# Kernel optimization log

Measured on AMD Instinct MI355X. Metric: run time of the kernel, lower is better.

The kernel has to match this reference:

```python
import jax, jax.numpy as jnp
import numpy as np

MAX_WEIGHT = 10.0  # config.max_weight
EPS = 1e-8

BATCH = 2048
VOCAB = 256
SEQ_LEN = 64
NUM_DENDRITES = SEQ_LEN * VOCAB  # 16384


def setup_inputs() -> dict:
    key = jax.random.key(0)
    k1, k2 = jax.random.split(key)
    # binary dendrite activations in {0,1}, stored as float32 as in the torch module
    binary = jax.random.randint(k1, (BATCH, NUM_DENDRITES), 0, 2).astype(jnp.float32)
    # raw_weights ~ Uniform(-1, 1) per nn.init.uniform_
    raw_weights = jax.random.uniform(k2, (VOCAB, NUM_DENDRITES), dtype=jnp.float32,
                                     minval=-1.0, maxval=1.0)
    return {"binary": binary, "raw_weights": raw_weights}


def reference(binary, raw_weights):
    # bounded positive weights: max_weight * sigmoid(raw)
    w = MAX_WEIGHT * jax.nn.sigmoid(raw_weights)            # (vocab, D)
    log_w = jnp.log(jnp.clip(w, EPS))                       # (vocab, D)
    # masked log-sum: where binary==0 the torch code uses log(1)=0, then multiplies
    # by binary anyway, so it is exactly binary @ log_w.T
    log_sum = jnp.einsum('bd,vd->bv', binary, log_w)        # (batch, vocab)
    n_active = jnp.clip(jnp.sum(binary, axis=-1, keepdims=True), 1.0)  # (batch, 1)
    logits = jnp.exp(log_sum / n_active)                    # geometric mean of fired weights
    return logits
```

## Files before the change

### kernel.cpp

```cpp
#include <hip/hip_runtime.h>

#define BATCH 2048
#define VOCAB 256
#define KDIM 16384
#define BM 64
#define BK 64
#define S_SPLIT 32
#define KCHUNK (KDIM / S_SPLIT)
#define NT (KCHUNK / BK)
#define LN10 2.302585092994046f

typedef __attribute__((ext_vector_type(8))) short short8;
typedef __attribute__((ext_vector_type(4))) float f32x4;

#define FENCE asm volatile("" ::: "memory")

__device__ __forceinline__ unsigned short f2bf_rne(float f) {
  unsigned int u = __float_as_uint(f);
  u += 0x7fffu + ((u >> 16) & 1u);
  return (unsigned short)(u >> 16);
}
__device__ __forceinline__ unsigned int pack2(float lo, float hi) {
  return (__float_as_uint(lo) >> 16) | (__float_as_uint(hi) & 0xffff0000u);
}

__device__ __forceinline__ void async16(void* lds, const void* g) {
  __builtin_amdgcn_global_load_lds(
      (const __attribute__((address_space(1))) unsigned int*)g,
      (__attribute__((address_space(3))) unsigned int*)lds, 16, 0, 0);
}

__global__ __launch_bounds__(256) void k_logw(const float* __restrict__ raw,
                                              unsigned short* __restrict__ logw) {
  int i = blockIdx.x * 256 + threadIdx.x;
  float4 x = ((const float4*)raw)[i];
  ushort4 r;
  r.x = f2bf_rne(LN10 - log1pf(expf(-x.x)));
  r.y = f2bf_rne(LN10 - log1pf(expf(-x.y)));
  r.z = f2bf_rne(LN10 - log1pf(expf(-x.z)));
  r.w = f2bf_rne(LN10 - log1pf(expf(-x.w)));
  ((ushort4*)logw)[i] = r;
}

template <int PART>
__global__ __launch_bounds__(256, 3) void k_gemm(
    const float* __restrict__ binary, const unsigned short* __restrict__ logw,
    float* __restrict__ outp, float* __restrict__ nactp) {
  __shared__ char smem[40960];
  char* const Asm = smem;
  char* const Bsm = smem + 8192;

  const int tid = threadIdx.x;
  const int wv = tid >> 6;
  const int lane = tid & 63;
  const int l15 = lane & 15;
  const int lhi = lane >> 4;
  const int sx = blockIdx.x;
  const int my = blockIdx.y;
  const int m0 = my * BM;
  const int k0 = sx * KCHUNK;

  const int ar = tid >> 2, ac = tid & 3;
  const float* asrc = binary + (size_t)(m0 + ar) * KDIM + k0 + ac * 16;
  const int ar7 = ar & 7;
  const int aw0 = ar * 128 + ((((ac * 2) ^ ar7) << 4));
  const int aw1 = ar * 128 + ((((ac * 2 + 1) ^ ar7) << 4));

  const unsigned short* bsrc =
      logw + (size_t)(wv * 64 + (lane >> 3)) * KDIM + k0 +
      (((lane & 7) ^ (lane >> 3)) << 3);

  const int rsw = (l15 & 7) << 4;

  f32x4 acc[4][4];
#pragma unroll
  for (int m = 0; m < 4; ++m)
#pragma unroll
    for (int n = 0; n < 4; ++n) acc[m][n] = f32x4{0.f, 0.f, 0.f, 0.f};
  float asum = 0.f;
  float4 Ra[4], Rb[4];

  auto ALOAD = [&](int t, float4* R) {
    const float4* p = (const float4*)(asrc + t * BK);
    R[0] = p[0]; R[1] = p[1]; R[2] = p[2]; R[3] = p[3];
  };
  auto BSTAGE = [&](int t) {
#pragma unroll
    for (int i = 0; i < 8; ++i)
      async16(Bsm + (wv * 64 + i * 8) * 128, bsrc + (size_t)i * 8 * KDIM + t * BK);
  };
  auto AWRITE = [&](const float4* R) {
#pragma unroll
    for (int j = 0; j < 4; ++j)
      asum += R[j].x + R[j].y + R[j].z + R[j].w;
    uint4 u0, u1;
    u0.x = pack2(R[0].x, R[0].y); u0.y = pack2(R[0].z, R[0].w);
    u0.z = pack2(R[1].x, R[1].y); u0.w = pack2(R[1].z, R[1].w);
    u1.x = pack2(R[2].x, R[2].y); u1.y = pack2(R[2].z, R[2].w);
    u1.z = pack2(R[3].x, R[3].y); u1.w = pack2(R[3].z, R[3].w);
    *(uint4*)(Asm + aw0) = u0;
    *(uint4*)(Asm + aw1) = u1;
  };
  auto COMPUTE = [&]() {
#pragma unroll
    for (int ks = 0; ks < 2; ++ks) {
      const int koff = ((ks * 64) | (lhi * 16)) ^ rsw;
      short8 af[4], bf[4];
#pragma unroll
      for (int m = 0; m < 4; ++m)
        af[m] = *(const short8*)(Asm + (m * 16 + l15) * 128 + koff);
#pragma unroll
      for (int n = 0; n < 4; ++n)
        bf[n] = *(const short8*)(Bsm + (wv * 64 + n * 16 + l15) * 128 + koff);
#pragma unroll
      for (int m = 0; m < 4; ++m)
#pragma unroll
        for (int n = 0; n < 4; ++n)
          acc[m][n] = __builtin_amdgcn_mfma_f32_16x16x32_bf16(bf[n], af[m],
                                                              acc[m][n], 0, 0, 0);
    }
  };

#define VMW4 asm volatile("s_waitcnt vmcnt(4) lgkmcnt(0)" ::: "memory")
#define BAR __builtin_amdgcn_s_barrier()

  ALOAD(0, Ra);
#pragma unroll 1
  for (int t = 0; t < NT; t += 2) {
    BSTAGE(t);
    AWRITE(Ra);
    ALOAD(t + 1, Rb);
    VMW4; BAR; FENCE;
    COMPUTE();
    FENCE; BAR; FENCE;
    BSTAGE(t + 1);
    AWRITE(Rb);
    ALOAD(t + 2 < NT ? t + 2 : NT - 1, Ra);
    VMW4; BAR; FENCE;
    COMPUTE();
    FENCE; BAR; FENCE;
  }

  float s = asum;
  s += __shfl_xor(s, 1, 64);
  s += __shfl_xor(s, 2, 64);

  if (PART) {
    if (ac == 0) nactp[sx * BATCH + m0 + ar] = s;
#pragma unroll
    for (int m = 0; m < 4; ++m) {
      float* dst = outp + ((size_t)sx * BATCH + m0 + m * 16 + l15) * VOCAB +
                   wv * 64 + lhi * 4;
#pragma unroll
      for (int n = 0; n < 4; ++n)
        *(float4*)(dst + n * 16) =
            (float4){acc[m][n][0], acc[m][n][1], acc[m][n][2], acc[m][n][3]};
    }
  } else {
    if (ac == 0) atomicAdd(&nactp[m0 + ar], s);
#pragma unroll
    for (int m = 0; m < 4; ++m)
#pragma unroll
      for (int n = 0; n < 4; ++n)
#pragma unroll
        for (int i = 0; i < 4; ++i)
          atomicAdd(&outp[(size_t)(m0 + m * 16 + l15) * VOCAB + wv * 64 +
                          n * 16 + lhi * 4 + i],
                    acc[m][n][i]);
  }
}

__global__ __launch_bounds__(256) void k_reduce(const float* __restrict__ part,
                                                const float* __restrict__ nactp,
                                                float* __restrict__ out) {
  int b = blockIdx.x;
  int v = threadIdx.x;
  float sum = 0.f, n = 0.f;
#pragma unroll
  for (int i = 0; i < S_SPLIT; ++i) {
    sum += part[((size_t)i * BATCH + b) * VOCAB + v];
    n += nactp[i * BATCH + b];
  }
  out[(size_t)b * VOCAB + v] = expf(sum / fmaxf(n, 1.f));
}

__global__ __launch_bounds__(256) void k_out(float* __restrict__ io,
                                             const float* __restrict__ nact) {
  int b = blockIdx.x;
  int v = threadIdx.x;
  float n = fmaxf(nact[b], 1.0f);
  size_t idx = (size_t)b * VOCAB + v;
  io[idx] = expf(io[idx] / n);
}

extern "C" void kernel_launch(void* const* d_in, const int* in_sizes, int n_in,
                              void* d_out, int out_size, void* d_ws, size_t ws_size,
                              hipStream_t stream) {
  const float* binary = (const float*)d_in[0];
  const float* raw = (const float*)d_in[1];
  float* out = (float*)d_out;
  char* ws = (char*)d_ws;

  const size_t LOGW_B = (size_t)VOCAB * KDIM * 2;
  const size_t NACT_B = (size_t)S_SPLIT * BATCH * 4;
  const size_t PART_B = (size_t)S_SPLIT * BATCH * VOCAB * 4;
  unsigned short* logw = (unsigned short*)ws;
  float* nactp = (float*)(ws + LOGW_B);
  float* part = (float*)(ws + LOGW_B + NACT_B);

  k_logw<<<(VOCAB * KDIM / 4) / 256, 256, 0, stream>>>(raw, logw);

  dim3 g(S_SPLIT, BATCH / BM);
  if (ws_size >= LOGW_B + NACT_B + PART_B) {
    k_gemm<1><<<g, 256, 0, stream>>>(binary, logw, part, nactp);
    k_reduce<<<BATCH, VOCAB, 0, stream>>>(part, nactp, out);
  } else {
    hipMemsetAsync(out, 0, (size_t)BATCH * VOCAB * sizeof(float), stream);
    hipMemsetAsync(nactp, 0, BATCH * sizeof(float), stream);
    k_gemm<0><<<g, 256, 0, stream>>>(binary, logw, out, nactp);
    k_out<<<BATCH, VOCAB, 0, stream>>>(out, nactp);
  }
}
```

Before: 262.7 us.

## Bit-pack binary activations in a pre-pass and expand via LDS lookup table

```diff
diff --git a/kernel.cpp b/kernel.cpp
--- a/kernel.cpp
+++ b/kernel.cpp
@@ -3,25 +3,27 @@
 #define BATCH 2048
 #define VOCAB 256
 #define KDIM 16384
+#define WPR (KDIM / 32)
 #define BM 64
 #define BK 64
-#define S_SPLIT 32
+#define S_SPLIT 16
 #define KCHUNK (KDIM / S_SPLIT)
 #define NT (KCHUNK / BK)
+#define CW (KCHUNK / 32)
 #define LN10 2.302585092994046f
 
 typedef __attribute__((ext_vector_type(8))) short short8;
 typedef __attribute__((ext_vector_type(4))) float f32x4;
 
 #define FENCE asm volatile("" ::: "memory")
+#define BAR __builtin_amdgcn_s_barrier()
+#define VMW8 asm volatile("s_waitcnt vmcnt(8)" ::: "memory")
+#define VMW0 asm volatile("s_waitcnt vmcnt(0)" ::: "memory")
 
 __device__ __forceinline__ unsigned short f2bf_rne(float f) {
   unsigned int u = __float_as_uint(f);
   u += 0x7fffu + ((u >> 16) & 1u);
   return (unsigned short)(u >> 16);
-}
-__device__ __forceinline__ unsigned int pack2(float lo, float hi) {
-  return (__float_as_uint(lo) >> 16) | (__float_as_uint(hi) & 0xffff0000u);
 }
 
 __device__ __forceinline__ void async16(void* lds, const void* g) {
@@ -42,13 +44,48 @@
   ((ushort4*)logw)[i] = r;
 }
 
+__global__ __launch_bounds__(256) void k_pack(const float* __restrict__ binary,
+                                              unsigned int* __restrict__ bits,
+                                              float* __restrict__ nact) {
+  const int r = blockIdx.x;
+  const int t = threadIdx.x;
+  const int lane = t & 63;
+  const float4* src = (const float4*)(binary + (size_t)r * KDIM);
+  unsigned int* wrow = bits + (size_t)r * WPR;
+  float cnt = 0.f;
+#pragma unroll
+  for (int i = 0; i < 16; ++i) {
+    float4 f = src[i * 256 + t];
+    unsigned int nib = ((__float_as_uint(f.x) >> 29) & 1u) |
+                       ((__float_as_uint(f.y) >> 28) & 2u) |
+                       ((__float_as_uint(f.z) >> 27) & 4u) |
+                       ((__float_as_uint(f.w) >> 26) & 8u);
+    unsigned int v = nib, p;
+    p = __shfl_xor(v, 1, 64); v = (lane & 1) ? (p | (v << 4)) : (v | (p << 4));
+    p = __shfl_xor(v, 2, 64); v = (lane & 2) ? (p | (v << 8)) : (v | (p << 8));
+    p = __shfl_xor(v, 4, 64); v = (lane & 4) ? (p | (v << 16)) : (v | (p << 16));
+    if ((t & 7) == 0) wrow[i * 32 + (t >> 3)] = v;
+    cnt += (float)__popc(v);
+  }
+  cnt *= 0.125f;
+  cnt += __shfl_xor(cnt, 1, 64);
+  cnt += __shfl_xor(cnt, 2, 64);
+  cnt += __shfl_xor(cnt, 4, 64);
+  cnt += __shfl_xor(cnt, 8, 64);
+  cnt += __shfl_xor(cnt, 16, 64);
+  cnt += __shfl_xor(cnt, 32, 64);
+  if (lane == 0) atomicAdd(&nact[r], cnt);
+}
+
 template <int PART>
-__global__ __launch_bounds__(256, 3) void k_gemm(
-    const float* __restrict__ binary, const unsigned short* __restrict__ logw,
-    float* __restrict__ outp, float* __restrict__ nactp) {
-  __shared__ char smem[40960];
-  char* const Asm = smem;
-  char* const Bsm = smem + 8192;
+__global__ __launch_bounds__(256) void k_gemm(
+    const unsigned int* __restrict__ bits, const unsigned short* __restrict__ logw,
+    float* __restrict__ outp) {
+  extern __shared__ char smem[];
+  char* const B0 = smem;
+  char* const B1 = smem + 32768;
+  unsigned int* const Wb = (unsigned int*)(smem + 65536);
+  uint4* const LUT = (uint4*)(smem + 74752);
 
   const int tid = threadIdx.x;
   const int wv = tid >> 6;
@@ -56,20 +93,30 @@
   const int l15 = lane & 15;
   const int lhi = lane >> 4;
   const int sx = blockIdx.x;
-  const int my = blockIdx.y;
-  const int m0 = my * BM;
+  const int m0 = blockIdx.y * BM;
   const int k0 = sx * KCHUNK;
 
-  const int ar = tid >> 2, ac = tid & 3;
-  const float* asrc = binary + (size_t)(m0 + ar) * KDIM + k0 + ac * 16;
-  const int ar7 = ar & 7;
-  const int aw0 = ar * 128 + ((((ac * 2) ^ ar7) << 4));
-  const int aw1 = ar * 128 + ((((ac * 2 + 1) ^ ar7) << 4));
+  {
+    unsigned int e0 = ((tid >> 0) & 1 ? 0x3F80u : 0u) | ((tid >> 1) & 1 ? 0x3F800000u : 0u);
+    unsigned int e1 = ((tid >> 2) & 1 ? 0x3F80u : 0u) | ((tid >> 3) & 1 ? 0x3F800000u : 0u);
+    unsigned int e2 = ((tid >> 4) & 1 ? 0x3F80u : 0u) | ((tid >> 5) & 1 ? 0x3F800000u : 0u);
+    unsigned int e3 = ((tid >> 6) & 1 ? 0x3F80u : 0u) | ((tid >> 7) & 1 ? 0x3F800000u : 0u);
+    LUT[tid] = (uint4){e0, e1, e2, e3};
+  }
+  {
+    const unsigned int* gsrc =
+        bits + (size_t)(m0 + (tid >> 2)) * WPR + sx * CW + (tid & 3) * 8;
+    uint4 w0 = *(const uint4*)gsrc;
+    uint4 w1 = *(const uint4*)(gsrc + 4);
+    unsigned int* ld = Wb + (tid >> 2) * 36 + (tid & 3) * 8;
+    *(uint4*)ld = w0;
+    *(uint4*)(ld + 4) = w1;
+  }
+  __syncthreads();
 
   const unsigned short* bsrc =
       logw + (size_t)(wv * 64 + (lane >> 3)) * KDIM + k0 +
       (((lane & 7) ^ (lane >> 3)) << 3);
-
   const int rsw = (l15 & 7) << 4;
 
   f32x4 acc[4][4];
@@ -77,76 +124,58 @@
   for (int m = 0; m < 4; ++m)
 #pragma unroll
     for (int n = 0; n < 4; ++n) acc[m][n] = f32x4{0.f, 0.f, 0.f, 0.f};
-  float asum = 0.f;
-  float4 Ra[4], Rb[4];
-
-  auto ALOAD = [&](int t, float4* R) {
-    const float4* p = (const float4*)(asrc + t * BK);
-    R[0] = p[0]; R[1] = p[1]; R[2] = p[2]; R[3] = p[3];
+
+  auto BSTAGE = [&](int t, char* B) {
+#pragma unroll
+    for (int i = 0; i < 8; ++i)
+      async16(B + (wv * 64 + i * 8) * 128, bsrc + (size_t)i * 8 * KDIM + t * BK);
   };
-  auto BSTAGE = [&](int t) {
-#pragma unroll
-    for (int i = 0; i < 8; ++i)
-      async16(Bsm + (wv * 64 + i * 8) * 128, bsrc + (size_t)i * 8 * KDIM + t * BK);
-  };
-  auto AWRITE = [&](const float4* R) {
-#pragma unroll
-    for (int j = 0; j < 4; ++j)
-      asum += R[j].x + R[j].y + R[j].z + R[j].w;
-    uint4 u0, u1;
-    u0.x = pack2(R[0].x, R[0].y); u0.y = pack2(R[0].z, R[0].w);
-    u0.z = pack2(R[1].x, R[1].y); u0.w = pack2(R[1].z, R[1].w);
-    u1.x = pack2(R[2].x, R[2].y); u1.y = pack2(R[2].z, R[2].w);
-    u1.z = pack2(R[3].x, R[3].y); u1.w = pack2(R[3].z, R[3].w);
-    *(uint4*)(Asm + aw0) = u0;
-    *(uint4*)(Asm + aw1) = u1;
-  };
-  auto COMPUTE = [&]() {
+  auto COMPUTE = [&](const char* B, int t) {
+    uint2 aw[4];
+#pragma unroll
+    for (int m = 0; m < 4; ++m)
+      aw[m] = *(const uint2*)(Wb + (m * 16 + l15) * 36 + 2 * t);
 #pragma unroll
     for (int ks = 0; ks < 2; ++ks) {
       const int koff = ((ks * 64) | (lhi * 16)) ^ rsw;
-      short8 af[4], bf[4];
-#pragma unroll
-      for (int m = 0; m < 4; ++m)
-        af[m] = *(const short8*)(Asm + (m * 16 + l15) * 128 + koff);
+      short8 bf[4];
 #pragma unroll
       for (int n = 0; n < 4; ++n)
-        bf[n] = *(const short8*)(Bsm + (wv * 64 + n * 16 + l15) * 128 + koff);
-#pragma unroll
-      for (int m = 0; m < 4; ++m)
+        bf[n] = *(const short8*)(B + (wv * 64 + n * 16 + l15) * 128 + koff);
+#pragma unroll
+      for (int m = 0; m < 4; ++m) {
+        unsigned int w = ks ? aw[m].y : aw[m].x;
+        unsigned int byt = (w >> (lhi * 8)) & 0xffu;
+        union { uint4 u; short8 s; } ex;
+        ex.u = LUT[byt];
 #pragma unroll
         for (int n = 0; n < 4; ++n)
-          acc[m][n] = __builtin_amdgcn_mfma_f32_16x16x32_bf16(bf[n], af[m],
+          acc[m][n] = __builtin_amdgcn_mfma_f32_16x16x32_bf16(bf[n], ex.s,
                                                               acc[m][n], 0, 0, 0);
+      }
     }
   };
 
-#define VMW4 asm volatile("s_waitcnt vmcnt(4) lgkmcnt(0)" ::: "memory")
-#define BAR __builtin_amdgcn_s_barrier()
-
-  ALOAD(0, Ra);
+  BSTAGE(0, B0);
+  FENCE;
 #pragma unroll 1
   for (int t = 0; t < NT; t += 2) {
-    BSTAGE(t);
-    AWRITE(Ra);
-    ALOAD(t + 1, Rb);
-    VMW4; BAR; FENCE;
-    COMPUTE();
+    BSTAGE(t + 1, B1);
+    FENCE; VMW8; BAR; FENCE;
+    COMPUTE(B0, t);
     FENCE; BAR; FENCE;
-    BSTAGE(t + 1);
-    AWRITE(Rb);
-    ALOAD(t + 2 < NT ? t + 2 : NT - 1, Ra);
-    VMW4; BAR; FENCE;
-    COMPUTE();
+    if (t + 2 < NT) {
+      BSTAGE(t + 2, B0);
+      FENCE; VMW8;
+    } else {
+      VMW0;
+    }
+    BAR; FENCE;
+    COMPUTE(B1, t + 1);
     FENCE; BAR; FENCE;
   }
 
-  float s = asum;
-  s += __shfl_xor(s, 1, 64);
-  s += __shfl_xor(s, 2, 64);
-
   if (PART) {
-    if (ac == 0) nactp[sx * BATCH + m0 + ar] = s;
 #pragma unroll
     for (int m = 0; m < 4; ++m) {
       float* dst = outp + ((size_t)sx * BATCH + m0 + m * 16 + l15) * VOCAB +
@@ -157,7 +186,6 @@
             (float4){acc[m][n][0], acc[m][n][1], acc[m][n][2], acc[m][n][3]};
     }
   } else {
-    if (ac == 0) atomicAdd(&nactp[m0 + ar], s);
 #pragma unroll
     for (int m = 0; m < 4; ++m)
 #pragma unroll
@@ -171,17 +199,15 @@
 }
 
 __global__ __launch_bounds__(256) void k_reduce(const float* __restrict__ part,
-                                                const float* __restrict__ nactp,
+                                                const float* __restrict__ nact,
                                                 float* __restrict__ out) {
   int b = blockIdx.x;
   int v = threadIdx.x;
-  float sum = 0.f, n = 0.f;
-#pragma unroll
-  for (int i = 0; i < S_SPLIT; ++i) {
+  float sum = 0.f;
+#pragma unroll
+  for (int i = 0; i < S_SPLIT; ++i)
     sum += part[((size_t)i * BATCH + b) * VOCAB + v];
-    n += nactp[i * BATCH + b];
-  }
-  out[(size_t)b * VOCAB + v] = expf(sum / fmaxf(n, 1.f));
+  out[(size_t)b * VOCAB + v] = expf(sum / fmaxf(nact[b], 1.f));
 }
 
 __global__ __launch_bounds__(256) void k_out(float* __restrict__ io,
@@ -202,22 +228,26 @@
   char* ws = (char*)d_ws;
 
   const size_t LOGW_B = (size_t)VOCAB * KDIM * 2;
-  const size_t NACT_B = (size_t)S_SPLIT * BATCH * 4;
+  const size_t BITS_B = (size_t)BATCH * WPR * 4;
+  const size_t NACT_B = (size_t)BATCH * 4;
   const size_t PART_B = (size_t)S_SPLIT * BATCH * VOCAB * 4;
   unsigned short* logw = (unsigned short*)ws;
-  float* nactp = (float*)(ws + LOGW_B);
-  float* part = (float*)(ws + LOGW_B + NACT_B);
-
+  unsigned int* bits = (unsigned int*)(ws + LOGW_B);
+  float* nact = (float*)(ws + LOGW_B + BITS_B);
+  float* part = (float*)(ws + LOGW_B + BITS_B + NACT_B);
+
+  hipMemsetAsync(nact, 0, NACT_B, stream);
   k_logw<<<(VOCAB * KDIM / 4) / 256, 256, 0, stream>>>(raw, logw);
+  k_pack<<<BATCH, 256, 0, stream>>>(binary, bits, nact);
 
   dim3 g(S_SPLIT, BATCH / BM);
-  if (ws_size >= LOGW_B + NACT_B + PART_B) {
-    k_gemm<1><<<g, 256, 0, stream>>>(binary, logw, part, nactp);
-    k_reduce<<<BATCH, VOCAB, 0, stream>>>(part, nactp, out);
+  const size_t LDS_B = 78848;
+  if (ws_size >= LOGW_B + BITS_B + NACT_B + PART_B) {
+    k_gemm<1><<<g, 256, LDS_B, stream>>>(bits, logw, part);
+    k_reduce<<<BATCH, VOCAB, 0, stream>>>(part, nact, out);
   } else {
     hipMemsetAsync(out, 0, (size_t)BATCH * VOCAB * sizeof(float), stream);
-    hipMemsetAsync(nactp, 0, BATCH * sizeof(float), stream);
-    k_gemm<0><<<g, 256, 0, stream>>>(binary, logw, out, nactp);
-    k_out<<<BATCH, VOCAB, 0, stream>>>(out, nactp);
-  }
-}
+    k_gemm<0><<<g, 256, LDS_B, stream>>>(bits, logw, out);
+    k_out<<<BATCH, VOCAB, 0, stream>>>(out, nact);
+  }
+}
```

Result: faster. 243.5 us (-7.3%).
